# Kernel optimization log

Measured on AMD Instinct MI355X. Metric: run time of the kernel, lower is better.

The kernel has to match this reference:

```python
import jax, jax.numpy as jnp
import numpy as np

N = 100_000
E = 1_600_000
D = 128
LN_EPS = 1e-5


def _gcn_layer(x, src, dst, W, b, gamma, beta):
    # GCNConv (PyG defaults): linear transform, add self-loops, symmetric norm,
    # scatter-add aggregation, then bias. Followed by LayerNorm + ReLU.
    n = x.shape[0]
    h = x @ W  # [N, out]
    loop = jnp.arange(n, dtype=src.dtype)
    src_f = jnp.concatenate([src, loop])  # [E+N]
    dst_f = jnp.concatenate([dst, loop])
    deg = jax.ops.segment_sum(jnp.ones(src_f.shape[0], dtype=h.dtype), dst_f, num_segments=n)
    dinv = jnp.where(deg > 0, jax.lax.rsqrt(deg), 0.0)
    norm = dinv[src_f] * dinv[dst_f]  # [E+N]
    msg = h[src_f] * norm[:, None]  # [E+N, out] -- dominant HBM traffic
    out = jax.ops.segment_sum(msg, dst_f, num_segments=n) + b
    # LayerNorm over feature dim
    mu = jnp.mean(out, axis=-1, keepdims=True)
    var = jnp.mean(jnp.square(out - mu), axis=-1, keepdims=True)
    ln = (out - mu) * jax.lax.rsqrt(var + LN_EPS) * gamma + beta
    # ReLU; dropout is identity in eval mode
    return jax.nn.relu(ln)


def setup_inputs() -> dict:
    key = jax.random.key(0)
    ks = jax.random.split(key, 10)
    x = jax.random.normal(ks[0], (N, D), dtype=jnp.float32)
    edge_index = jax.random.randint(ks[1], (2, E), 0, N, dtype=jnp.int32)
    s = 1.0 / np.sqrt(D)
    W1 = jax.random.normal(ks[2], (D, D), dtype=jnp.float32) * s
    b1 = jnp.zeros((D,), dtype=jnp.float32)
    g1 = jnp.ones((D,), dtype=jnp.float32)
    be1 = jnp.zeros((D,), dtype=jnp.float32)
    W2 = jax.random.normal(ks[3], (D, D), dtype=jnp.float32) * s
    b2 = jnp.zeros((D,), dtype=jnp.float32)
    g2 = jnp.ones((D,), dtype=jnp.float32)
    be2 = jnp.zeros((D,), dtype=jnp.float32)
    return {"x": x, "edge_index": edge_index, "W1": W1, "b1": b1, "g1": g1,
            "be1": be1, "W2": W2, "b2": b2, "g2": g2, "be2": be2}


def reference(x, edge_index, W1, b1, g1, be1, W2, b2, g2, be2):
    src, dst = edge_index[0], edge_index[1]  # PyG flow: source_to_target
    h = _gcn_layer(x, src, dst, W1, b1, g1, be1)
    h = _gcn_layer(h, src, dst, W2, b2, g2, be2)
    return h
```

## Files before the change

kernel.cpp:

```cpp
#include <hip/hip_runtime.h>

#define D 128
#define NBSHIFT 10
#define NB (1 << NBSHIFT)
#define EPB 2048

typedef __attribute__((ext_vector_type(8))) short bf16x8;
typedef __attribute__((ext_vector_type(4))) float floatx4;

__device__ __forceinline__ float bflo(unsigned int u){ return __uint_as_float(u << 16); }
__device__ __forceinline__ float bfhi(unsigned int u){ return __uint_as_float(u & 0xffff0000u); }
__device__ __forceinline__ unsigned int f2bfbits(float f){
    unsigned int x = __float_as_uint(f);
    return (x + 0x7fffu + ((x >> 16) & 1u)) >> 16;
}

__global__ __launch_bounds__(256) void k_bcount(const int* __restrict__ dst, int* __restrict__ bcnt, int E){
    __shared__ int hist[128];
    int t = threadIdx.x;
    int base = blockIdx.x * EPB;
    if (t < 128) hist[t] = 0;
    __syncthreads();
#pragma unroll
    for (int j = 0; j < 8; ++j){
        int e = base + j * 256 + t;
        if (e < E) atomicAdd(&hist[dst[e] >> NBSHIFT], 1);
    }
    __syncthreads();
    if (t < 128 && hist[t] > 0) atomicAdd(&bcnt[t], hist[t]);
}

__global__ void k_bscan(const int* __restrict__ bcnt, int* __restrict__ bbase, int* __restrict__ bcur,
                        int* __restrict__ rowStartN, int NBK){
    if (threadIdx.x == 0){
        int run = 0;
        for (int b = 0; b < NBK; ++b){ bbase[b] = run; bcur[b] = run; run += bcnt[b]; }
        bbase[NBK] = run;
        *rowStartN = run;
    }
}

__global__ __launch_bounds__(256) void k_bucket(const int* __restrict__ src, const int* __restrict__ dst,
                                                int* __restrict__ bcur, unsigned int* __restrict__ edge1,
                                                int NBK, int E){
    __shared__ int hist[128], lstart[128], lcur[128], gbase[128];
    __shared__ unsigned int stage[EPB];
    int t = threadIdx.x;
    int base = blockIdx.x * EPB;
    int tot = min(EPB, E - base);
    if (t < 128) hist[t] = 0;
    __syncthreads();

    unsigned int ent[8]; int bk[8]; int cnt = 0;
#pragma unroll
    for (int j = 0; j < 8; ++j){
        int e = base + j * 256 + t;
        if (e < base + tot){
            unsigned s = (unsigned)src[e], d = (unsigned)dst[e];
            ent[cnt] = s | ((d & (NB - 1)) << 20);
            bk[cnt] = (int)(d >> NBSHIFT);
            atomicAdd(&hist[bk[cnt]], 1);
            ++cnt;
        }
    }
    __syncthreads();
    if (t < 128) lstart[t] = hist[t];
    __syncthreads();
    for (int off = 1; off < 128; off <<= 1){
        int v = 0;
        if (t < 128 && t >= off) v = lstart[t - off];
        __syncthreads();
        if (t < 128) lstart[t] += v;
        __syncthreads();
    }
    if (t < 128){
        int ex = lstart[t] - hist[t];
        lstart[t] = ex;
        lcur[t] = ex;
        if (t < NBK && hist[t] > 0) gbase[t] = atomicAdd(&bcur[t], hist[t]);
    }
    __syncthreads();
    for (int j = 0; j < cnt; ++j){
        int pos = atomicAdd(&lcur[bk[j]], 1);
        stage[pos] = ent[j];
    }
    __syncthreads();
    for (int i = t; i < tot; i += 256){
        unsigned int e1 = stage[i];
        int b = (int)((e1 >> 20) & (NB - 1));
        int lo = 0, hi = 127;
        while (lo < hi){
            int midb = (lo + hi + 1) >> 1;
            if (lstart[midb] <= i) lo = midb; else hi = midb - 1;
        }
        b = lo;
        edge1[gbase[b] + (i - lstart[b])] = e1;
    }
}

__global__ __launch_bounds__(1024) void k_csr2(const unsigned int* __restrict__ edge1,
                                               const int* __restrict__ bbase,
                                               int* __restrict__ rowStart, float* __restrict__ dinv,
                                               int* __restrict__ csr, int N){
    __shared__ int hist[NB];
    __shared__ int sc[NB];
    int b = blockIdx.x, t = threadIdx.x;
    int nbase = b << NBSHIFT;
    int nn = min(N - nbase, NB);
    int ebeg = bbase[b], eend = bbase[b + 1];

    if (t < NB) hist[t] = 0;
    __syncthreads();
    for (int i = ebeg + t; i < eend; i += 1024)
        atomicAdd(&hist[edge1[i] >> 20], 1);
    __syncthreads();
    if (t < NB) sc[t] = hist[t];
    __syncthreads();
    for (int off = 1; off < NB; off <<= 1){
        int v = (t >= off && t < NB) ? sc[t - off] : 0;
        __syncthreads();
        if (t < NB) sc[t] += v;
        __syncthreads();
    }
    if (t < NB){
        int cur = ebeg + sc[t] - hist[t];
        sc[t] = cur;
        if (t < nn){
            rowStart[nbase + t] = cur;
            dinv[nbase + t] = rsqrtf((float)hist[t] + 1.0f);
        }
    }
    __syncthreads();
    for (int i = ebeg + t; i < eend; i += 1024){
        unsigned int p = edge1[i];
        int pos = atomicAdd(&sc[p >> 20], 1);
        csr[pos] = (int)(p & 0xFFFFFu);
    }
}

__global__ __launch_bounds__(256) void k_wtrans(const float* __restrict__ W1,
                                                const float* __restrict__ W2,
                                                unsigned short* __restrict__ Wt1,
                                                unsigned short* __restrict__ Wt2){
    int i = blockIdx.x * 256 + threadIdx.x;
    const float* Ws; unsigned short* Wd; int j = i;
    if (i < 16384){ Ws = W1; Wd = Wt1; } else { Ws = W2; Wd = Wt2; j -= 16384; }
    int k = j >> 7, n = j & 127;
    Wd[n * 128 + k] = (unsigned short)f2bfbits(Ws[k * 128 + n]);
}

template<bool A_BF16>
__global__ __launch_bounds__(256) void k_gemm(const void* __restrict__ Av,
                                              const unsigned short* __restrict__ Wt,
                                              unsigned short* __restrict__ Hout, int Nrows){
    int wave = threadIdx.x >> 6, lane = threadIdx.x & 63;
    int m = lane & 15, quad = lane >> 4;
    int row0 = blockIdx.x * 64 + wave * 16;
    int arow = row0 + m;
    int arowc = arow < Nrows ? arow : Nrows - 1;

    bf16x8 a[4];
    if (A_BF16){
        const unsigned short* Ap = (const unsigned short*)Av + (size_t)arowc * D + quad * 8;
#pragma unroll
        for (int kt = 0; kt < 4; ++kt) a[kt] = *(const bf16x8*)(Ap + kt * 32);
    } else {
        const float* Ap = (const float*)Av + (size_t)arowc * D + quad * 8;
#pragma unroll
        for (int kt = 0; kt < 4; ++kt){
            float4 v0 = *(const float4*)(Ap + kt * 32);
            float4 v1 = *(const float4*)(Ap + kt * 32 + 4);
            bf16x8 af;
            af[0] = (short)f2bfbits(v0.x); af[1] = (short)f2bfbits(v0.y);
            af[2] = (short)f2bfbits(v0.z); af[3] = (short)f2bfbits(v0.w);
            af[4] = (short)f2bfbits(v1.x); af[5] = (short)f2bfbits(v1.y);
            af[6] = (short)f2bfbits(v1.z); af[7] = (short)f2bfbits(v1.w);
            a[kt] = af;
        }
    }

    floatx4 acc[8];
#pragma unroll
    for (int nt = 0; nt < 8; ++nt) acc[nt] = (floatx4){0.f, 0.f, 0.f, 0.f};

    const unsigned short* Bp = Wt + m * D + quad * 8;
#pragma unroll
    for (int kt = 0; kt < 4; ++kt){
        bf16x8 bk[8];
#pragma unroll
        for (int nt = 0; nt < 8; ++nt) bk[nt] = *(const bf16x8*)(Bp + nt * 16 * D + kt * 32);
#pragma unroll
        for (int nt = 0; nt < 8; ++nt)
            acc[nt] = __builtin_amdgcn_mfma_f32_16x16x32_bf16(a[kt], bk[nt], acc[nt], 0, 0, 0);
    }
#pragma unroll
    for (int nt = 0; nt < 8; ++nt){
#pragma unroll
        for (int r = 0; r < 4; ++r){
            int rr = row0 + quad * 4 + r;
            if (rr < Nrows) Hout[(size_t)rr * D + nt * 16 + m] = (unsigned short)f2bfbits(acc[nt][r]);
        }
    }
}

template<bool OUT_BF16>
__global__ __launch_bounds__(256) void k_agg(const unsigned short* __restrict__ h,
                                             const int* __restrict__ rowStart,
                                             const int* __restrict__ csr,
                                             const float* __restrict__ dinv,
                                             const float* __restrict__ bias,
                                             const float* __restrict__ gamma,
                                             const float* __restrict__ beta,
                                             void* __restrict__ outv, int N){
    int node = blockIdx.x * 4 + (threadIdx.x >> 6);
    if (node >= N) return;
    int lane = threadIdx.x & 63;
    int half = lane >> 5, li = lane & 31;
    const uint2* hv = (const uint2*)h;

    float dv = dinv[node];
    float4 acc = {0.f, 0.f, 0.f, 0.f};
    if (half == 0){
        uint2 hs = hv[(size_t)node * 32 + li];
        float w0 = dv * dv;
        acc.x = bflo(hs.x) * w0; acc.y = bfhi(hs.x) * w0;
        acc.z = bflo(hs.y) * w0; acc.w = bfhi(hs.y) * w0;
    }

    int start = rowStart[node], end = rowStart[node + 1];
    int mid = start + ((end - start + 1) >> 1);
    int i    = half ? mid : start;
    int iend = half ? end : mid;

    for (; i + 4 <= iend; i += 4){
        int s0 = csr[i], s1 = csr[i + 1], s2 = csr[i + 2], s3 = csr[i + 3];
        uint2 h0 = hv[(size_t)s0 * 32 + li];
        uint2 h1 = hv[(size_t)s1 * 32 + li];
        uint2 h2 = hv[(size_t)s2 * 32 + li];
        uint2 h3 = hv[(size_t)s3 * 32 + li];
        float w0 = dinv[s0] * dv, w1 = dinv[s1] * dv, w2 = dinv[s2] * dv, w3 = dinv[s3] * dv;
        acc.x = fmaf(bflo(h0.x), w0, acc.x); acc.y = fmaf(bfhi(h0.x), w0, acc.y);
        acc.z = fmaf(bflo(h0.y), w0, acc.z); acc.w = fmaf(bfhi(h0.y), w0, acc.w);
        acc.x = fmaf(bflo(h1.x), w1, acc.x); acc.y = fmaf(bfhi(h1.x), w1, acc.y);
        acc.z = fmaf(bflo(h1.y), w1, acc.z); acc.w = fmaf(bfhi(h1.y), w1, acc.w);
        acc.x = fmaf(bflo(h2.x), w2, acc.x); acc.y = fmaf(bfhi(h2.x), w2, acc.y);
        acc.z = fmaf(bflo(h2.y), w2, acc.z); acc.w = fmaf(bfhi(h2.y), w2, acc.w);
        acc.x = fmaf(bflo(h3.x), w3, acc.x); acc.y = fmaf(bfhi(h3.x), w3, acc.y);
        acc.z = fmaf(bflo(h3.y), w3, acc.z); acc.w = fmaf(bfhi(h3.y), w3, acc.w);
    }
    for (; i < iend; ++i){
        int s = csr[i];
        float ws = dinv[s] * dv;
        uint2 hs = hv[(size_t)s * 32 + li];
        acc.x = fmaf(bflo(hs.x), ws, acc.x); acc.y = fmaf(bfhi(hs.x), ws, acc.y);
        acc.z = fmaf(bflo(hs.y), ws, acc.z); acc.w = fmaf(bfhi(hs.y), ws, acc.w);
    }

    acc.x += __shfl_xor(acc.x, 32, 64);
    acc.y += __shfl_xor(acc.y, 32, 64);
    acc.z += __shfl_xor(acc.z, 32, 64);
    acc.w += __shfl_xor(acc.w, 32, 64);

    float4 bb = ((const float4*)bias)[li];
    acc.x += bb.x; acc.y += bb.y; acc.z += bb.z; acc.w += bb.w;

    float s1 = acc.x + acc.y + acc.z + acc.w;
    float s2 = acc.x * acc.x + acc.y * acc.y + acc.z * acc.z + acc.w * acc.w;
#pragma unroll
    for (int off = 16; off > 0; off >>= 1){
        s1 += __shfl_xor(s1, off, 64);
        s2 += __shfl_xor(s2, off, 64);
    }
    float mu = s1 * (1.0f / 128.0f);
    float var = s2 * (1.0f / 128.0f) - mu * mu;
    float rstd = rsqrtf(var + 1e-5f);

    float4 gg = ((const float4*)gamma)[li];
    float4 be = ((const float4*)beta)[li];
    float ox = fmaxf(fmaf((acc.x - mu) * rstd, gg.x, be.x), 0.0f);
    float oy = fmaxf(fmaf((acc.y - mu) * rstd, gg.y, be.y), 0.0f);
    float oz = fmaxf(fmaf((acc.z - mu) * rstd, gg.z, be.z), 0.0f);
    float ow = fmaxf(fmaf((acc.w - mu) * rstd, gg.w, be.w), 0.0f);
    if (half == 0){
        if (OUT_BF16){
            uint2 o;
            o.x = f2bfbits(ox) | (f2bfbits(oy) << 16);
            o.y = f2bfbits(oz) | (f2bfbits(ow) << 16);
            ((uint2*)outv)[(size_t)node * 32 + li] = o;
        } else {
            floatx4 o = {ox, oy, oz, ow};
            __builtin_nontemporal_store(o, (floatx4*)outv + (size_t)node * 32 + li);
        }
    }
}

extern "C" void kernel_launch(void* const* d_in, const int* in_sizes, int n_in,
                              void* d_out, int out_size, void* d_ws, size_t ws_size,
                              hipStream_t stream){
    const float* x   = (const float*)d_in[0];
    const int*   ei  = (const int*)d_in[1];
    const float* W1  = (const float*)d_in[2];
    const float* b1  = (const float*)d_in[3];
    const float* g1  = (const float*)d_in[4];
    const float* be1 = (const float*)d_in[5];
    const float* W2  = (const float*)d_in[6];
    const float* b2  = (const float*)d_in[7];
    const float* g2  = (const float*)d_in[8];
    const float* be2 = (const float*)d_in[9];
    float* out = (float*)d_out;

    const int N = in_sizes[0] / D;
    const int E = in_sizes[1] / 2;
    const int* src = ei;
    const int* dst = ei + E;

    char* w = (char*)d_ws;
    size_t off = 0;
    auto alloc = [&](size_t bytes) -> char* {
        char* p = w + off;
        off = (off + bytes + 255) & ~(size_t)255;
        return p;
    };
    const int NBK = (N + NB - 1) >> NBSHIFT;
    int*            bcnt     = (int*)alloc((size_t)NBK * 4);
    int*            bbase    = (int*)alloc((size_t)(NBK + 1) * 4);
    int*            bcur     = (int*)alloc((size_t)NBK * 4);
    int*            rowStart = (int*)alloc((size_t)(N + 1) * 4);
    float*          dinv     = (float*)alloc((size_t)N * 4);
    unsigned int*   edge1    = (unsigned int*)alloc((size_t)E * 4);
    int*            csr      = (int*)alloc((size_t)E * 4);
    unsigned short* wt1      = (unsigned short*)alloc(16384 * 2);
    unsigned short* wt2      = (unsigned short*)alloc(16384 * 2);
    unsigned short* h        = (unsigned short*)alloc((size_t)N * D * 2);
    unsigned short* hmid     = (unsigned short*)d_out;

    (void)hipMemsetAsync(bcnt, 0, (size_t)NBK * 4, stream);

    int gB = (E + EPB - 1) / EPB;
    int gG = (N + 63) / 64;
    int gA = (N + 3) / 4;

    k_bcount<<<gB, 256, 0, stream>>>(dst, bcnt, E);
    k_bscan <<<1, 64, 0, stream>>>(bcnt, bbase, bcur, rowStart + N, NBK);
    k_bucket<<<gB, 256, 0, stream>>>(src, dst, bcur, edge1, NBK, E);
    k_csr2  <<<NBK, 1024, 0, stream>>>(edge1, bbase, rowStart, dinv, csr, N);
    k_wtrans<<<128, 256, 0, stream>>>(W1, W2, wt1, wt2);

    k_gemm<false><<<gG, 256, 0, stream>>>(x, wt1, h, N);
    k_agg<true>  <<<gA, 256, 0, stream>>>(h, rowStart, csr, dinv, b1, g1, be1, hmid, N);
    k_gemm<true> <<<gG, 256, 0, stream>>>(hmid, wt2, h, N);
    k_agg<false> <<<gA, 256, 0, stream>>>(h, rowStart, csr, dinv, b2, g2, be2, out, N);
}
```

Before: 413.4 us.

## Replace bucketed two-pass CSR build with global-atomic degree count and scatter

Replaces the bucket-sort CSR construction (block histograms, bucket scatter through shared staging, per-bucket local sort) with a direct approach: global atomic degree counting, a three-kernel prefix scan, and a global-atomic scatter of source indices into CSR slots. This removes the intermediate edge1 array and its extra pass. In exchange it relies on many contended global atomics on random destinations and random-address writes. The order of neighbours within a row also becomes nondeterministic, which can change float summation order.

```diff
diff --git a/kernel.cpp b/kernel.cpp
--- a/kernel.cpp
+++ b/kernel.cpp
@@ -1,9 +1,6 @@
 #include <hip/hip_runtime.h>
 
 #define D 128
-#define NBSHIFT 10
-#define NB (1 << NBSHIFT)
-#define EPB 2048
 
 typedef __attribute__((ext_vector_type(8))) short bf16x8;
 typedef __attribute__((ext_vector_type(4))) float floatx4;
@@ -15,126 +12,70 @@
     return (x + 0x7fffu + ((x >> 16) & 1u)) >> 16;
 }
 
-__global__ __launch_bounds__(256) void k_bcount(const int* __restrict__ dst, int* __restrict__ bcnt, int E){
-    __shared__ int hist[128];
+__global__ __launch_bounds__(256) void k_deg(const int* __restrict__ dst, int* __restrict__ deg, int E){
+    int base = blockIdx.x * 2048 + threadIdx.x;
+#pragma unroll
+    for (int j = 0; j < 8; ++j){
+        int e = base + j * 256;
+        if (e < E) atomicAdd(&deg[dst[e]], 1);
+    }
+}
+
+__global__ __launch_bounds__(1024) void k_scan1(const int* __restrict__ deg, int* __restrict__ rowStart,
+                                                int* __restrict__ bsum, int N){
+    __shared__ int sc[1024];
+    int t = threadIdx.x, i = blockIdx.x * 1024 + t;
+    int v = (i < N) ? deg[i] : 0;
+    sc[t] = v;
+    __syncthreads();
+    for (int off = 1; off < 1024; off <<= 1){
+        int u = (t >= off) ? sc[t - off] : 0;
+        __syncthreads();
+        sc[t] += u;
+        __syncthreads();
+    }
+    if (i < N) rowStart[i] = sc[t] - v;
+    if (t == 1023) bsum[blockIdx.x] = sc[1023];
+}
+
+__global__ __launch_bounds__(1024) void k_scan2(int* __restrict__ bsum, int* __restrict__ rowStartN, int C){
+    __shared__ int sc[1024];
     int t = threadIdx.x;
-    int base = blockIdx.x * EPB;
-    if (t < 128) hist[t] = 0;
+    int v = (t < C) ? bsum[t] : 0;
+    sc[t] = v;
     __syncthreads();
+    for (int off = 1; off < 1024; off <<= 1){
+        int u = (t >= off) ? sc[t - off] : 0;
+        __syncthreads();
+        sc[t] += u;
+        __syncthreads();
+    }
+    if (t < C) bsum[t] = sc[t] - v;
+    if (t == 1023) *rowStartN = sc[1023];
+}
+
+__global__ __launch_bounds__(1024) void k_scan3(const int* __restrict__ deg, const int* __restrict__ bsum,
+                                                int* __restrict__ rowStart, int* __restrict__ cur,
+                                                float* __restrict__ dinv, int N){
+    int i = blockIdx.x * 1024 + threadIdx.x;
+    if (i < N){
+        int r = rowStart[i] + bsum[blockIdx.x];
+        rowStart[i] = r;
+        cur[i] = r;
+        dinv[i] = rsqrtf((float)deg[i] + 1.0f);
+    }
+}
+
+__global__ __launch_bounds__(256) void k_scatter(const int* __restrict__ src, const int* __restrict__ dst,
+                                                 int* __restrict__ cur, int* __restrict__ csr, int E){
+    int base = blockIdx.x * 2048 + threadIdx.x;
 #pragma unroll
     for (int j = 0; j < 8; ++j){
-        int e = base + j * 256 + t;
-        if (e < E) atomicAdd(&hist[dst[e] >> NBSHIFT], 1);
-    }
-    __syncthreads();
-    if (t < 128 && hist[t] > 0) atomicAdd(&bcnt[t], hist[t]);
-}
-
-__global__ void k_bscan(const int* __restrict__ bcnt, int* __restrict__ bbase, int* __restrict__ bcur,
-                        int* __restrict__ rowStartN, int NBK){
-    if (threadIdx.x == 0){
-        int run = 0;
-        for (int b = 0; b < NBK; ++b){ bbase[b] = run; bcur[b] = run; run += bcnt[b]; }
-        bbase[NBK] = run;
-        *rowStartN = run;
-    }
-}
-
-__global__ __launch_bounds__(256) void k_bucket(const int* __restrict__ src, const int* __restrict__ dst,
-                                                int* __restrict__ bcur, unsigned int* __restrict__ edge1,
-                                                int NBK, int E){
-    __shared__ int hist[128], lstart[128], lcur[128], gbase[128];
-    __shared__ unsigned int stage[EPB];
-    int t = threadIdx.x;
-    int base = blockIdx.x * EPB;
-    int tot = min(EPB, E - base);
-    if (t < 128) hist[t] = 0;
-    __syncthreads();
-
-    unsigned int ent[8]; int bk[8]; int cnt = 0;
-#pragma unroll
-    for (int j = 0; j < 8; ++j){
-        int e = base + j * 256 + t;
-        if (e < base + tot){
-            unsigned s = (unsigned)src[e], d = (unsigned)dst[e];
-            ent[cnt] = s | ((d & (NB - 1)) << 20);
-            bk[cnt] = (int)(d >> NBSHIFT);
-            atomicAdd(&hist[bk[cnt]], 1);
-            ++cnt;
-        }
-    }
-    __syncthreads();
-    if (t < 128) lstart[t] = hist[t];
-    __syncthreads();
-    for (int off = 1; off < 128; off <<= 1){
-        int v = 0;
-        if (t < 128 && t >= off) v = lstart[t - off];
-        __syncthreads();
-        if (t < 128) lstart[t] += v;
-        __syncthreads();
-    }
-    if (t < 128){
-        int ex = lstart[t] - hist[t];
-        lstart[t] = ex;
-        lcur[t] = ex;
-        if (t < NBK && hist[t] > 0) gbase[t] = atomicAdd(&bcur[t], hist[t]);
-    }
-    __syncthreads();
-    for (int j = 0; j < cnt; ++j){
-        int pos = atomicAdd(&lcur[bk[j]], 1);
-        stage[pos] = ent[j];
-    }
-    __syncthreads();
-    for (int i = t; i < tot; i += 256){
-        unsigned int e1 = stage[i];
-        int b = (int)((e1 >> 20) & (NB - 1));
-        int lo = 0, hi = 127;
-        while (lo < hi){
-            int midb = (lo + hi + 1) >> 1;
-            if (lstart[midb] <= i) lo = midb; else hi = midb - 1;
-        }
-        b = lo;
-        edge1[gbase[b] + (i - lstart[b])] = e1;
-    }
-}
-
-__global__ __launch_bounds__(1024) void k_csr2(const unsigned int* __restrict__ edge1,
-                                               const int* __restrict__ bbase,
-                                               int* __restrict__ rowStart, float* __restrict__ dinv,
-                                               int* __restrict__ csr, int N){
-    __shared__ int hist[NB];
-    __shared__ int sc[NB];
-    int b = blockIdx.x, t = threadIdx.x;
-    int nbase = b << NBSHIFT;
-    int nn = min(N - nbase, NB);
-    int ebeg = bbase[b], eend = bbase[b + 1];
-
-    if (t < NB) hist[t] = 0;
-    __syncthreads();
-    for (int i = ebeg + t; i < eend; i += 1024)
-        atomicAdd(&hist[edge1[i] >> 20], 1);
-    __syncthreads();
-    if (t < NB) sc[t] = hist[t];
-    __syncthreads();
-    for (int off = 1; off < NB; off <<= 1){
-        int v = (t >= off && t < NB) ? sc[t - off] : 0;
-        __syncthreads();
-        if (t < NB) sc[t] += v;
-        __syncthreads();
-    }
-    if (t < NB){
-        int cur = ebeg + sc[t] - hist[t];
-        sc[t] = cur;
-        if (t < nn){
-            rowStart[nbase + t] = cur;
-            dinv[nbase + t] = rsqrtf((float)hist[t] + 1.0f);
-        }
-    }
-    __syncthreads();
-    for (int i = ebeg + t; i < eend; i += 1024){
-        unsigned int p = edge1[i];
-        int pos = atomicAdd(&sc[p >> 20], 1);
-        csr[pos] = (int)(p & 0xFFFFFu);
+        int e = base + j * 256;
+        if (e < E){
+            int pos = atomicAdd(&cur[dst[e]], 1);
+            csr[pos] = src[e];
+        }
     }
 }
 
@@ -321,30 +262,30 @@
         off = (off + bytes + 255) & ~(size_t)255;
         return p;
     };
-    const int NBK = (N + NB - 1) >> NBSHIFT;
-    int*            bcnt     = (int*)alloc((size_t)NBK * 4);
-    int*            bbase    = (int*)alloc((size_t)(NBK + 1) * 4);
-    int*            bcur     = (int*)alloc((size_t)NBK * 4);
+    const int C = (N + 1023) >> 10;
+    int*            deg      = (int*)alloc((size_t)N * 4);
+    int*            bsum     = (int*)alloc((size_t)C * 4);
     int*            rowStart = (int*)alloc((size_t)(N + 1) * 4);
+    int*            cur      = (int*)alloc((size_t)N * 4);
     float*          dinv     = (float*)alloc((size_t)N * 4);
-    unsigned int*   edge1    = (unsigned int*)alloc((size_t)E * 4);
     int*            csr      = (int*)alloc((size_t)E * 4);
     unsigned short* wt1      = (unsigned short*)alloc(16384 * 2);
     unsigned short* wt2      = (unsigned short*)alloc(16384 * 2);
     unsigned short* h        = (unsigned short*)alloc((size_t)N * D * 2);
     unsigned short* hmid     = (unsigned short*)d_out;
 
-    (void)hipMemsetAsync(bcnt, 0, (size_t)NBK * 4, stream);
-
-    int gB = (E + EPB - 1) / EPB;
+    (void)hipMemsetAsync(deg, 0, (size_t)N * 4, stream);
+
+    int gE = (E + 2047) / 2048;
     int gG = (N + 63) / 64;
     int gA = (N + 3) / 4;
 
-    k_bcount<<<gB, 256, 0, stream>>>(dst, bcnt, E);
-    k_bscan <<<1, 64, 0, stream>>>(bcnt, bbase, bcur, rowStart + N, NBK);
-    k_bucket<<<gB, 256, 0, stream>>>(src, dst, bcur, edge1, NBK, E);
-    k_csr2  <<<NBK, 1024, 0, stream>>>(edge1, bbase, rowStart, dinv, csr, N);
-    k_wtrans<<<128, 256, 0, stream>>>(W1, W2, wt1, wt2);
+    k_deg    <<<gE, 256, 0, stream>>>(dst, deg, E);
+    k_scan1  <<<C, 1024, 0, stream>>>(deg, rowStart, bsum, N);
+    k_scan2  <<<1, 1024, 0, stream>>>(bsum, rowStart + N, C);
+    k_scan3  <<<C, 1024, 0, stream>>>(deg, bsum, rowStart, cur, dinv, N);
+    k_scatter<<<gE, 256, 0, stream>>>(src, dst, cur, csr, E);
+    k_wtrans <<<128, 256, 0, stream>>>(W1, W2, wt1, wt2);
 
     k_gemm<false><<<gG, 256, 0, stream>>>(x, wt1, h, N);
     k_agg<true>  <<<gA, 256, 0, stream>>>(h, rowStart, csr, dinv, b1, g1, be1, hmid, N);
```

Result: slower. 565.6 us (+36.8%).
